# Kernel optimization log

Hardware: AMD Instinct MI355X
Metric: run time of the kernel (lower is better)

The kernel has to match this reference:

```python
import jax, jax.numpy as jnp
import numpy as np

# TT structure: W is [in_features, out_features] = [4096, 4096]
IN_FACTORS = (16, 16, 16)
OUT_FACTORS = (16, 16, 16)
RANKS = (1, 8, 8, 1)
BATCH = 8192
IN_FEATURES = 4096
OUT_FEATURES = 4096
ITER_NUM = 3
L = 1.0
S = -1.0
EPSILON = 1.0


def tt_dense_matmul(cores, mat):
    """Multiply TT-matrix (cores[k]: [r_{k-1}, m_k, n_k, r_k]) by dense mat [prod(n), P].
    Returns [prod(m), P]. Sequential core contractions, never materializes dense W."""
    P = mat.shape[1]
    data = mat.reshape(1, mat.shape[0], P)  # [r=1, N_rem, T]
    M = 1
    for core in cores:
        r0, m, n, r1 = core.shape
        nrem = data.shape[1]
        d4 = data.reshape(r0, n, nrem // n, -1)            # [r0, n_k, N_rem', T]
        data = jnp.einsum('rmns,rnat->satm', core, d4)      # [r1, N_rem', T, m_k]
        data = data.reshape(r1, nrem // n, -1)              # fold m_k into trailing T
        M *= m
    return data.reshape(P, M).T  # [M, P]


def tt_tt_mul(cores_a, cores_b):
    """TT-matrix product: cores of A [M,K] and B [K,N] -> cores of A@B with Kronecker ranks."""
    out = []
    for ca, cb in zip(cores_a, cores_b):
        a0, m, n, a1 = ca.shape
        b0, n2, l, b1 = cb.shape
        c = jnp.einsum('amnb,cnld->acmlbd', ca, cb)
        out.append(c.reshape(a0 * b0, m, l, a1 * b1))
    return out


def setup_inputs() -> dict:
    key = jax.random.key(0)
    ks = jax.random.split(key, 5)
    x = jax.random.normal(ks[0], (BATCH, IN_FEATURES), dtype=jnp.float32)
    # TT cores of weight W [in, out]: core_k shape [r_{k-1}, in_k, out_k, r_k]
    core_std = 0.3  # glorot-like per-core scale
    cores = []
    for k in range(3):
        shp = (RANKS[k], IN_FACTORS[k], OUT_FACTORS[k], RANKS[k + 1])
        cores.append(core_std * jax.random.normal(ks[k + 1], shp, dtype=jnp.float32))
    bias = 0.01 * jnp.ones((OUT_FEATURES,), dtype=jnp.float32)
    return {"x": x, "core0": cores[0], "core1": cores[1], "core2": cores[2], "bias": bias}


def reference(x, core0, core1, core2, bias):
    cores = [core0, core1, core2]
    # weight_t = t3.transpose(weight): swap in/out mode of each core
    cores_t = [c.transpose(0, 2, 1, 3) for c in cores]  # W^T: [out, in]
    x_t = x.T  # [in, B]
    mv = tt_dense_matmul(cores_t, x_t).T  # x @ W, [B, out]
    # norm-gated shrinkage init
    norm_x = jnp.linalg.norm(x)
    x_l = (mv + bias) / L + jnp.where(norm_x > EPSILON, 0.0, S)
    # G = W^T @ W in TT form (ranks grow to 64)
    G = tt_tt_mul(cores_t, cores)
    for _ in range(1, ITER_NUM):
        nrm = jnp.linalg.norm(x_l)
        term = tt_dense_matmul(G, x_l.T).T  # x_l @ (W^T W), [B, out]
        x_l = x_l - term / L + mv / L + bias + jnp.where(nrm > EPSILON, 0.0, S)
    return x_l
```

## Files before the change

### kernel.cpp

```cpp
#include <hip/hip_runtime.h>
#include <stdint.h>

typedef __bf16 bf16;
typedef __bf16 bf16x4 __attribute__((ext_vector_type(4)));
typedef __bf16 bf16x8 __attribute__((ext_vector_type(8)));
typedef float f32x4 __attribute__((ext_vector_type(4)));

#define GLD_LDS16(g, l)                                                        \
  __builtin_amdgcn_global_load_lds(                                            \
      (const __attribute__((address_space(1))) void*)(g),                      \
      (__attribute__((address_space(3))) void*)(l), 16, 0, 0)

#define BAR() asm volatile("s_barrier" ::: "memory")
#define VMW(n) asm volatile("s_waitcnt vmcnt(" #n ")" ::: "memory")
#define PRIO(x) __builtin_amdgcn_s_setprio(x)

__global__ __launch_bounds__(256) void k_pre(
    const float* __restrict__ x, const float* __restrict__ c0,
    const float* __restrict__ c1, const float* __restrict__ c2,
    bf16* __restrict__ Wt, bf16* __restrict__ xb, float* __restrict__ pbuf,
    float* __restrict__ g0, float* __restrict__ g1, float* __restrict__ g2) {
  const int b = blockIdx.x;
  if (b < 4096) {
    const int j = b;
    const int j0 = j >> 8, j1 = (j >> 4) & 15, j2 = j & 15;
    const int t = threadIdx.x;
    const int i0 = t >> 4, i1 = t & 15;
    float t0[8];
    {
      float4 v0 = *(const float4*)&c0[(i0 * 16 + j0) * 8];
      float4 v1 = *(const float4*)&c0[(i0 * 16 + j0) * 8 + 4];
      t0[0] = v0.x; t0[1] = v0.y; t0[2] = v0.z; t0[3] = v0.w;
      t0[4] = v1.x; t0[5] = v1.y; t0[6] = v1.z; t0[7] = v1.w;
    }
    float a[8];
#pragma unroll
    for (int r2 = 0; r2 < 8; ++r2) a[r2] = 0.f;
#pragma unroll
    for (int r1 = 0; r1 < 8; ++r1) {
      const float* row = &c1[((r1 * 16 + i1) * 16 + j1) * 8];
      float4 u0 = *(const float4*)row;
      float4 u1 = *(const float4*)(row + 4);
      a[0] += t0[r1] * u0.x; a[1] += t0[r1] * u0.y;
      a[2] += t0[r1] * u0.z; a[3] += t0[r1] * u0.w;
      a[4] += t0[r1] * u1.x; a[5] += t0[r1] * u1.y;
      a[6] += t0[r1] * u1.z; a[7] += t0[r1] * u1.w;
    }
    union { bf16 h[16]; bf16x8 v[2]; } u;
#pragma unroll
    for (int i2 = 0; i2 < 16; ++i2) {
      float s = 0.f;
#pragma unroll
      for (int r2 = 0; r2 < 8; ++r2) s += a[r2] * c2[(r2 * 16 + i2) * 16 + j2];
      u.h[i2] = (bf16)s;
    }
    bf16* dst = Wt + (size_t)j * 4096 + i0 * 256 + i1 * 16;
    ((bf16x8*)dst)[0] = u.v[0];
    ((bf16x8*)dst)[1] = u.v[1];
  } else if (b < 5120) {
    const int n4 = 8192 * 4096 / 4;
    int tid = (b - 4096) * 256 + threadIdx.x;
    const int stride = 1024 * 256;
    const float4* x4 = (const float4*)x;
    bf16x4* xb4 = (bf16x4*)xb;
    float acc = 0.f;
    for (int i = tid; i < n4; i += stride) {
      float4 v = x4[i];
      acc += v.x * v.x + v.y * v.y + v.z * v.z + v.w * v.w;
      bf16x4 bb;
      bb.x = (bf16)v.x; bb.y = (bf16)v.y; bb.z = (bf16)v.z; bb.w = (bf16)v.w;
      xb4[i] = bb;
    }
#pragma unroll
    for (int off = 32; off; off >>= 1) acc += __shfl_down(acc, off);
    __shared__ float red[4];
    if ((threadIdx.x & 63) == 0) red[threadIdx.x >> 6] = acc;
    __syncthreads();
    if (threadIdx.x == 0) pbuf[b - 4096] = red[0] + red[1] + red[2] + red[3];
  } else {
    int tid = (b - 5120) * 256 + threadIdx.x;
    if (tid < 16384) {
      int jj = tid >> 6, p1 = tid & 63;
      int j0 = jj >> 4, j0p = jj & 15, r1 = p1 >> 3, r1p = p1 & 7;
      float s = 0.f;
#pragma unroll
      for (int i0 = 0; i0 < 16; ++i0)
        s += c0[(i0 * 16 + j0) * 8 + r1] * c0[(i0 * 16 + j0p) * 8 + r1p];
      g0[tid] = s;
    } else if (tid < 32768) {
      int k = tid - 16384;
      int p2 = k >> 8, jj = k & 255;
      int r2 = p2 >> 3, r2p = p2 & 7, j2 = jj >> 4, j2p = jj & 15;
      float s = 0.f;
#pragma unroll
      for (int i2 = 0; i2 < 16; ++i2)
        s += c2[(r2 * 16 + i2) * 16 + j2] * c2[(r2p * 16 + i2) * 16 + j2p];
      g2[k] = s;
    } else {
      int k = tid - 32768;
      int p2 = k & 63, rest = k >> 6;
      int j1p = rest & 15, j1 = (rest >> 4) & 15, p1 = rest >> 8;
      int r1 = p1 >> 3, r1p = p1 & 7, r2 = p2 >> 3, r2p = p2 & 7;
      float s = 0.f;
#pragma unroll
      for (int i1 = 0; i1 < 16; ++i1)
        s += c1[((r1 * 16 + i1) * 16 + j1) * 8 + r2] *
             c1[((r1p * 16 + i1) * 16 + j1p) * 8 + r2p];
      g1[k] = s;
    }
  }
}

__global__ __launch_bounds__(256) void k_buildG(const float* __restrict__ g0,
                                                const float* __restrict__ g1,
                                                const float* __restrict__ g2,
                                                bf16* __restrict__ G,
                                                const float* __restrict__ pbuf,
                                                float* __restrict__ scal) {
  __shared__ float s_g2[16384];
  __shared__ float s_g1[4096];
  __shared__ float s_g0m[16384];
  const int t = threadIdx.x;

  if (blockIdx.x == 0) {
    float a = pbuf[t * 4] + pbuf[t * 4 + 1] + pbuf[t * 4 + 2] + pbuf[t * 4 + 3];
#pragma unroll
    for (int off = 32; off; off >>= 1) a += __shfl_down(a, off);
    if ((t & 63) == 0) s_g1[t >> 6] = a;
    __syncthreads();
    if (t == 0) {
      scal[0] = s_g1[0] + s_g1[1] + s_g1[2] + s_g1[3];
      scal[1] = 0.f; scal[2] = 0.f;
    }
    __syncthreads();
  }

  const int j1 = blockIdx.x >> 4, j1p = blockIdx.x & 15;
  const int jj1 = j1 * 16 + j1p;

  const float4* g2f4 = (const float4*)g2;
  float4* sg2f4 = (float4*)s_g2;
  for (int k = t; k < 4096; k += 256) sg2f4[k] = g2f4[k];
  const float4* g1f4 = (const float4*)g1;
  float4* sg1f4 = (float4*)s_g1;
  for (int k = t; k < 1024; k += 256) {
    int p1 = k >> 4, q = k & 15;
    sg1f4[k] = g1f4[(p1 * 256 + jj1) * 16 + q];
  }
#pragma unroll
  for (int q = 0; q < 16; ++q) {
    float4 v = ((const float4*)g0)[t * 16 + q];
    s_g0m[(q * 4 + 0) * 256 + t] = v.x;
    s_g0m[(q * 4 + 1) * 256 + t] = v.y;
    s_g0m[(q * 4 + 2) * 256 + t] = v.z;
    s_g0m[(q * 4 + 3) * 256 + t] = v.w;
  }
  __syncthreads();

  float m[64];
#pragma unroll
  for (int i = 0; i < 64; ++i) m[i] = 0.f;
#pragma unroll 4
  for (int p1 = 0; p1 < 64; ++p1) {
    float av = s_g0m[p1 * 256 + t];
#pragma unroll
    for (int q = 0; q < 16; ++q) {
      float4 v = ((const float4*)s_g1)[p1 * 16 + q];
      m[q * 4 + 0] += av * v.x; m[q * 4 + 1] += av * v.y;
      m[q * 4 + 2] += av * v.z; m[q * 4 + 3] += av * v.w;
    }
  }
  __syncthreads();
#pragma unroll
  for (int p2 = 0; p2 < 64; ++p2) s_g0m[p2 * 256 + t] = m[p2];
  __syncthreads();

  const int bcol = (t & 15) * 16;
  const int j2 = t & 15;
#pragma unroll 1
  for (int rep = 0; rep < 2; ++rep) {
    const int r0 = (((t >> 4) + rep * 16)) * 8;
    float acc2[8][16];
#pragma unroll
    for (int i = 0; i < 8; ++i)
#pragma unroll
      for (int c = 0; c < 16; ++c) acc2[i][c] = 0.f;
#pragma unroll 2
    for (int p2 = 0; p2 < 64; ++p2) {
      float4 mv0 = *(const float4*)&s_g0m[p2 * 256 + r0];
      float4 mv1 = *(const float4*)&s_g0m[p2 * 256 + r0 + 4];
      float mv[8] = {mv0.x, mv0.y, mv0.z, mv0.w, mv1.x, mv1.y, mv1.z, mv1.w};
      float gv[16];
#pragma unroll
      for (int q = 0; q < 4; ++q) {
        float4 v = *(const float4*)&s_g2[p2 * 256 + bcol + q * 4];
        gv[q * 4 + 0] = v.x; gv[q * 4 + 1] = v.y;
        gv[q * 4 + 2] = v.z; gv[q * 4 + 3] = v.w;
      }
#pragma unroll
      for (int i = 0; i < 8; ++i)
#pragma unroll
        for (int c = 0; c < 16; ++c) acc2[i][c] += mv[i] * gv[c];
    }
#pragma unroll
    for (int i = 0; i < 8; ++i) {
      const int jj0 = r0 + i;
      const int j0 = jj0 >> 4, j0p = jj0 & 15;
      bf16* d = G + (size_t)(j0 * 256 + j1 * 16 + j2) * 4096 + (j0p * 256 + j1p * 16);
      union { bf16 h[16]; bf16x8 v[2]; } u;
#pragma unroll
      for (int c = 0; c < 16; ++c) u.h[c] = (bf16)acc2[i][c];
      ((bf16x8*)d)[0] = u.v[0];
      ((bf16x8*)d)[1] = u.v[1];
    }
  }
}

#define STAGE_A(h, kt, b)                                                              \
  do {                                                                                 \
    GLD_LDS16(srcA + (size_t)((h) * 128) * K + (kt) * 64,                              \
              smem + (b) * 65536 + (h) * 16384 + wofs);                                \
    GLD_LDS16(srcA + (size_t)((h) * 128 + 64) * K + (kt) * 64,                         \
              smem + (b) * 65536 + (h) * 16384 + 8192 + wofs);                         \
  } while (0)
#define STAGE_B(h, kt, b)                                                              \
  do {                                                                                 \
    GLD_LDS16(srcB + (size_t)((h) * 128) * K + (kt) * 64,                              \
              smem + (b) * 65536 + 32768 + (h) * 16384 + wofs);                        \
    GLD_LDS16(srcB + (size_t)((h) * 128 + 64) * K + (kt) * 64,                         \
              smem + (b) * 65536 + 32768 + (h) * 16384 + 8192 + wofs);                 \
  } while (0)
#define LDA(ms, b)                                                                     \
  do {                                                                                 \
    const char* s_ = smem + (b) * 65536 + (ms) * 16384 + aRow;                         \
    _Pragma("unroll") for (int mi_ = 0; mi_ < 4; ++mi_) {                              \
      af[mi_][0] = *(const bf16x8*)(s_ + mi_ * 2048 + cb0);                            \
      af[mi_][1] = *(const bf16x8*)(s_ + mi_ * 2048 + cb1);                            \
    }                                                                                  \
  } while (0)
#define LDB(ns, b)                                                                     \
  do {                                                                                 \
    const char* s_ = smem + (b) * 65536 + 32768 + (ns) * 16384 + bRow;                 \
    _Pragma("unroll") for (int ni_ = 0; ni_ < 2; ++ni_) {                              \
      bfr[ns][ni_][0] = *(const bf16x8*)(s_ + ni_ * 2048 + cb0);                       \
      bfr[ns][ni_][1] = *(const bf16x8*)(s_ + ni_ * 2048 + cb1);                       \
    }                                                                                  \
  } while (0)
#define MQ(ms, ns)                                                                     \
  do {                                                                                 \
    PRIO(1);                                                                           \
    _Pragma("unroll") for (int mi_ = 0; mi_ < 4; ++mi_)                                \
    _Pragma("unroll") for (int ni_ = 0; ni_ < 2; ++ni_)                                \
    _Pragma("unroll") for (int ks_ = 0; ks_ < 2; ++ks_)                                \
        acc[(ms) * 4 + mi_][(ns) * 2 + ni_] =                                          \
            __builtin_amdgcn_mfma_f32_16x16x32_bf16(                                   \
                af[mi_][ks_], bfr[ns][ni_][ks_],                                       \
                acc[(ms) * 4 + mi_][(ns) * 2 + ni_], 0, 0, 0);                         \
    PRIO(0);                                                                           \
  } while (0)

__device__ __forceinline__ void run_core(const bf16* __restrict__ Ag,
                                         const bf16* __restrict__ Bg, const int K,
                                         const int bx, const int by, char* smem,
                                         f32x4 (&acc)[8][4]) {
  const int t = threadIdx.x;
  const int w = t >> 6, lane = t & 63;
  const int q = lane >> 4, lr = lane & 15;
  const int wm = w & 1, wn = w >> 1;

  const int r0 = t >> 3;
  const int ksrc = (t & 7) ^ (r0 & 7);
  const bf16* srcA = Ag + (size_t)(by * 256 + r0) * K + ksrc * 8;
  const bf16* srcB = Bg + (size_t)(bx * 256 + r0) * K + ksrc * 8;
  const int wofs = w << 10;

  const int aRow = (wm * 64 + lr) * 128;
  const int bRow = (wn * 32 + lr) * 128;
  const int cb0 = ((q ^ (lr & 7)) << 4);
  const int cb1 = (((4 + q) ^ (lr & 7)) << 4);

#pragma unroll
  for (int i = 0; i < 8; ++i)
#pragma unroll
    for (int j = 0; j < 4; ++j) acc[i][j] = (f32x4){0.f, 0.f, 0.f, 0.f};

  bf16x8 af[4][2];
  bf16x8 bfr[2][2][2];

  STAGE_A(0, 0, 0); STAGE_B(0, 0, 0); STAGE_B(1, 0, 0); STAGE_A(1, 0, 0);
  STAGE_A(0, 1, 1); STAGE_B(0, 1, 1); STAGE_B(1, 1, 1);
  VMW(6);
  BAR();

  const int NT = K >> 6;
#pragma unroll 1
  for (int tt = 0; tt + 3 < NT; tt += 2) {
    STAGE_A(1, tt + 1, 1);
    LDB(0, 0); LDA(0, 0); LDB(1, 0);
    MQ(0, 0); MQ(0, 1);
    BAR();
    STAGE_A(0, tt + 2, 0); STAGE_B(0, tt + 2, 0); STAGE_B(1, tt + 2, 0);
    LDA(1, 0);
    MQ(1, 1); MQ(1, 0);
    VMW(6);
    BAR();
    STAGE_A(1, tt + 2, 0);
    LDB(0, 1); LDA(0, 1); LDB(1, 1);
    MQ(0, 0); MQ(0, 1);
    BAR();
    STAGE_A(0, tt + 3, 1); STAGE_B(0, tt + 3, 1); STAGE_B(1, tt + 3, 1);
    LDA(1, 1);
    MQ(1, 1); MQ(1, 0);
    VMW(6);
    BAR();
  }

  STAGE_A(1, NT - 1, 1);
  LDB(0, 0); LDA(0, 0); LDB(1, 0);
  MQ(0, 0); MQ(0, 1);
  BAR();
  LDA(1, 0);
  MQ(1, 1); MQ(1, 0);
  VMW(0);
  BAR();
  LDB(0, 1); LDA(0, 1); LDB(1, 1);
  MQ(0, 0); MQ(0, 1);
  BAR();
  LDA(1, 1);
  MQ(1, 1); MQ(1, 0);
}

template <int MODE>
__global__ __launch_bounds__(512, 2) void k_gemm(
    const bf16* __restrict__ A, const bf16* __restrict__ Bt, int M, int N, int K,
    const float* __restrict__ bias, const bf16* __restrict__ xl0,
    const bf16* __restrict__ xl_prev, float* f32_out, bf16* __restrict__ bf_out,
    const float* __restrict__ ssq_a, const float* __restrict__ ssq_b,
    float* __restrict__ ssq_out) {
  const int nb = gridDim.x * gridDim.y;
  const int lin = blockIdx.y * gridDim.x + blockIdx.x;
  const int sw = (lin & 7) * (nb >> 3) + (lin >> 3);
  const int bx = sw % gridDim.x, by = sw / gridDim.x;
  __shared__ char smem[131072];

  float gate = 0.f;
  if constexpr (MODE == 0) {
    gate = (*ssq_a > 1.0f) ? 0.f : -1.f;
  } else {
    float g0v = (*ssq_a > 1.0f) ? 0.f : -1.f;
    float gtv = (*ssq_b > 1.0f) ? 0.f : -1.f;
    gate = gtv - g0v;
  }
  VMW(0);

  f32x4 acc[8][4];
  run_core(A, Bt, K, bx, by, smem, acc);

  const int t = threadIdx.x;
  const int w = t >> 6, lane = t & 63;
  const int q = lane >> 4, lr = lane & 15;
  const int wm = w & 1, wn = w >> 1;
  float ssql = 0.f;
#pragma unroll
  for (int mi = 0; mi < 8; ++mi) {
    const int grow = by * 256 + ((mi & 4) ? 128 : 0) + wm * 64 + (mi & 3) * 16 + q * 4;
#pragma unroll
    for (int r = 0; r < 4; ++r) {
      const size_t rowb = (size_t)(grow + r) * N;
#pragma unroll
      for (int ni = 0; ni < 4; ++ni) {
        const int gcol = bx * 256 + ((ni & 2) ? 128 : 0) + wn * 32 + (ni & 1) * 16 + lr;
        const size_t idx = rowb + gcol;
        float v = acc[mi][ni][r];
        if constexpr (MODE == 0) {
          float xl = v + bias[gcol] + gate;
          bf_out[idx] = (bf16)xl;
          ssql += xl * xl;
        } else if constexpr (MODE == 2) {
          float xl = 2.0f * (float)xl0[idx] - v + gate;
          bf_out[idx] = (bf16)xl;
          ssql += xl * xl;
        } else {
          f32_out[idx] = (float)xl_prev[idx] - v + (float)xl0[idx] + gate;
        }
      }
    }
  }
  if constexpr (MODE == 0 || MODE == 2) {
#pragma unroll
    for (int off = 32; off; off >>= 1) ssql += __shfl_down(ssql, off);
    __syncthreads();
    float* red = (float*)smem;
    if (lane == 0) red[w] = ssql;
    __syncthreads();
    if (t == 0) {
      float s = 0.f;
#pragma unroll
      for (int i = 0; i < 8; ++i) s += red[i];
      atomicAdd(ssq_out, s);
    }
  }
}

extern "C" void kernel_launch(void* const* d_in, const int* in_sizes, int n_in,
                              void* d_out, int out_size, void* d_ws, size_t ws_size,
                              hipStream_t stream) {
  const float* x = (const float*)d_in[0];
  const float* c0 = (const float*)d_in[1];
  const float* c1 = (const float*)d_in[2];
  const float* c2 = (const float*)d_in[3];
  const float* bias = (const float*)d_in[4];
  float* out = (float*)d_out;

  const int B = 8192, F = 4096;
  char* ws = (char*)d_ws;
  float* scal = (float*)ws;
  bf16* xbf = (bf16*)(ws + 256);
  bf16* Wt = (bf16*)(ws + 256 + (size_t)67108864);
  bf16* G = (bf16*)(ws + 256 + (size_t)100663296);
  bf16* xl0 = (bf16*)(ws + 256 + (size_t)134217728);
  bf16* xl1 = xbf;
  float* g0 = (float*)xl0;
  float* g2 = g0 + 16384;
  float* g1 = g2 + 16384;
  float* pbuf = g1 + 1048576;

  k_pre<<<9344, 256, 0, stream>>>(x, c0, c1, c2, Wt, xbf, pbuf, g0, g1, g2);
  k_buildG<<<256, 256, 0, stream>>>(g0, g1, g2, G, pbuf, scal);

  dim3 g1d(F / 256, B / 256);
  k_gemm<0><<<g1d, 512, 0, stream>>>(xbf, Wt, B, F, F, bias, nullptr, nullptr,
                                     nullptr, xl0, &scal[0], nullptr, &scal[1]);
  k_gemm<2><<<g1d, 512, 0, stream>>>(xl0, G, B, F, F, nullptr, xl0, nullptr,
                                     nullptr, xl1, &scal[0], &scal[1], &scal[2]);
  k_gemm<3><<<g1d, 512, 0, stream>>>(xl1, G, B, F, F, nullptr, xl0, xl1,
                                     out, nullptr, &scal[0], &scal[2], nullptr);
}
```

Baseline: 951.2 us.

## Restructure GEMM main loop into k-half register double-buffered pipeline

```diff
diff --git a/kernel.cpp b/kernel.cpp
--- a/kernel.cpp
+++ b/kernel.cpp
@@ -13,6 +13,7 @@
 
 #define BAR() asm volatile("s_barrier" ::: "memory")
 #define VMW(n) asm volatile("s_waitcnt vmcnt(" #n ")" ::: "memory")
+#define LGKM0() asm volatile("s_waitcnt lgkmcnt(0)" ::: "memory")
 #define PRIO(x) __builtin_amdgcn_s_setprio(x)
 
 __global__ __launch_bounds__(256) void k_pre(
@@ -230,32 +231,30 @@
     GLD_LDS16(srcB + (size_t)((h) * 128 + 64) * K + (kt) * 64,                         \
               smem + (b) * 65536 + 32768 + (h) * 16384 + 8192 + wofs);                 \
   } while (0)
-#define LDA(ms, b)                                                                     \
+#define STAGET(kt, b)                                                                  \
+  do { STAGE_A(0, kt, b); STAGE_A(1, kt, b); STAGE_B(0, kt, b); STAGE_B(1, kt, b); } while (0)
+#define LDQ(SA, SB, b, CB)                                                             \
   do {                                                                                 \
-    const char* s_ = smem + (b) * 65536 + (ms) * 16384 + aRow;                         \
-    _Pragma("unroll") for (int mi_ = 0; mi_ < 4; ++mi_) {                              \
-      af[mi_][0] = *(const bf16x8*)(s_ + mi_ * 2048 + cb0);                            \
-      af[mi_][1] = *(const bf16x8*)(s_ + mi_ * 2048 + cb1);                            \
-    }                                                                                  \
+    const char* As_ = smem + (b) * 65536 + aRow;                                       \
+    const char* Bs_ = smem + (b) * 65536 + 32768 + bRow;                               \
+    _Pragma("unroll") for (int ms_ = 0; ms_ < 2; ++ms_)                                \
+    _Pragma("unroll") for (int mi_ = 0; mi_ < 4; ++mi_)                                \
+        SA[ms_][mi_] = *(const bf16x8*)(As_ + ms_ * 16384 + mi_ * 2048 + (CB));        \
+    _Pragma("unroll") for (int ns_ = 0; ns_ < 2; ++ns_)                                \
+    _Pragma("unroll") for (int ni_ = 0; ni_ < 2; ++ni_)                                \
+        SB[ns_][ni_] = *(const bf16x8*)(Bs_ + ns_ * 16384 + ni_ * 2048 + (CB));        \
   } while (0)
-#define LDB(ns, b)                                                                     \
-  do {                                                                                 \
-    const char* s_ = smem + (b) * 65536 + 32768 + (ns) * 16384 + bRow;                 \
-    _Pragma("unroll") for (int ni_ = 0; ni_ < 2; ++ni_) {                              \
-      bfr[ns][ni_][0] = *(const bf16x8*)(s_ + ni_ * 2048 + cb0);                       \
-      bfr[ns][ni_][1] = *(const bf16x8*)(s_ + ni_ * 2048 + cb1);                       \
-    }                                                                                  \
-  } while (0)
-#define MQ(ms, ns)                                                                     \
+#define MQQ(SA, SB)                                                                    \
   do {                                                                                 \
     PRIO(1);                                                                           \
+    _Pragma("unroll") for (int ms_ = 0; ms_ < 2; ++ms_)                                \
     _Pragma("unroll") for (int mi_ = 0; mi_ < 4; ++mi_)                                \
+    _Pragma("unroll") for (int ns_ = 0; ns_ < 2; ++ns_)                                \
     _Pragma("unroll") for (int ni_ = 0; ni_ < 2; ++ni_)                                \
-    _Pragma("unroll") for (int ks_ = 0; ks_ < 2; ++ks_)                                \
-        acc[(ms) * 4 + mi_][(ns) * 2 + ni_] =                                          \
+        acc[ms_ * 4 + mi_][ns_ * 2 + ni_] =                                            \
             __builtin_amdgcn_mfma_f32_16x16x32_bf16(                                   \
-                af[mi_][ks_], bfr[ns][ni_][ks_],                                       \
-                acc[(ms) * 4 + mi_][(ns) * 2 + ni_], 0, 0, 0);                         \
+                SA[ms_][mi_], SB[ns_][ni_],                                            \
+                acc[ms_ * 4 + mi_][ns_ * 2 + ni_], 0, 0, 0);                           \
     PRIO(0);                                                                           \
   } while (0)
 
@@ -284,50 +283,49 @@
 #pragma unroll
     for (int j = 0; j < 4; ++j) acc[i][j] = (f32x4){0.f, 0.f, 0.f, 0.f};
 
-  bf16x8 af[4][2];
-  bf16x8 bfr[2][2][2];
-
-  STAGE_A(0, 0, 0); STAGE_B(0, 0, 0); STAGE_B(1, 0, 0); STAGE_A(1, 0, 0);
-  STAGE_A(0, 1, 1); STAGE_B(0, 1, 1); STAGE_B(1, 1, 1);
-  VMW(6);
+  bf16x8 a0[2][4], b0[2][2];
+  bf16x8 a1[2][4], b1[2][2];
+
+  STAGET(0, 0); STAGET(1, 1);
+  VMW(8);
   BAR();
-
-  const int NT = K >> 6;
-#pragma unroll 1
-  for (int tt = 0; tt + 3 < NT; tt += 2) {
-    STAGE_A(1, tt + 1, 1);
-    LDB(0, 0); LDA(0, 0); LDB(1, 0);
-    MQ(0, 0); MQ(0, 1);
-    BAR();
-    STAGE_A(0, tt + 2, 0); STAGE_B(0, tt + 2, 0); STAGE_B(1, tt + 2, 0);
-    LDA(1, 0);
-    MQ(1, 1); MQ(1, 0);
-    VMW(6);
-    BAR();
-    STAGE_A(1, tt + 2, 0);
-    LDB(0, 1); LDA(0, 1); LDB(1, 1);
-    MQ(0, 0); MQ(0, 1);
-    BAR();
-    STAGE_A(0, tt + 3, 1); STAGE_B(0, tt + 3, 1); STAGE_B(1, tt + 3, 1);
-    LDA(1, 1);
-    MQ(1, 1); MQ(1, 0);
-    VMW(6);
-    BAR();
-  }
-
-  STAGE_A(1, NT - 1, 1);
-  LDB(0, 0); LDA(0, 0); LDB(1, 0);
-  MQ(0, 0); MQ(0, 1);
-  BAR();
-  LDA(1, 0);
-  MQ(1, 1); MQ(1, 0);
+  LDQ(a0, b0, 0, cb0);
+  LGKM0();
   VMW(0);
   BAR();
-  LDB(0, 1); LDA(0, 1); LDB(1, 1);
-  MQ(0, 0); MQ(0, 1);
-  BAR();
-  LDA(1, 1);
-  MQ(1, 1); MQ(1, 0);
+  LDQ(a1, b1, 0, cb1);
+  MQQ(a0, b0);
+  LGKM0(); BAR();
+  LDQ(a0, b0, 1, cb0);
+  MQQ(a1, b1);
+  LGKM0(); BAR();
+
+#pragma unroll 1
+  for (int T = 1; T <= 61; T += 2) {
+    STAGET(T + 1, 0);
+    LDQ(a1, b1, 1, cb1);
+    MQQ(a0, b0);
+    LGKM0();
+    VMW(0);
+    BAR();
+    LDQ(a0, b0, 0, cb0);
+    MQQ(a1, b1);
+    LGKM0(); BAR();
+    STAGET(T + 2, 1);
+    LDQ(a1, b1, 0, cb1);
+    MQQ(a0, b0);
+    LGKM0();
+    VMW(0);
+    BAR();
+    LDQ(a0, b0, 1, cb0);
+    MQQ(a1, b1);
+    LGKM0(); BAR();
+  }
+
+  LDQ(a1, b1, 1, cb1);
+  MQQ(a0, b0);
+  LGKM0();
+  MQQ(a1, b1);
 }
 
 template <int MODE>
```

Result: slower. 2.216 ms (+133.0%).
